# Kernel tuning notes

Measured on AMD Instinct MI355X. Metric: run time of the kernel, lower is better.

Reference implementation:

```python
import jax, jax.numpy as jnp
import numpy as np

SEQ, B, IN, H = 512, 256, 300, 256

def setup_inputs() -> dict:
    key = jax.random.key(0)
    ks = jax.random.split(key, 14)
    s = lambda *sh: 1.0 / np.sqrt(sh[0])
    inp = {
        'secuencia': jax.random.normal(ks[0], (SEQ, B, IN), jnp.float32),
        # RNN cell 1 (forward direction)
        'W1x': jax.random.normal(ks[1], (IN, H), jnp.float32) * s(IN),
        'W1h': jax.random.normal(ks[2], (H, H), jnp.float32) * s(H),
        'b1':  jax.random.normal(ks[3], (H,), jnp.float32) * 0.01,
        # RNN cell 2 (backward direction)
        'W2x': jax.random.normal(ks[4], (IN, H), jnp.float32) * s(IN),
        'W2h': jax.random.normal(ks[5], (H, H), jnp.float32) * s(H),
        'b2':  jax.random.normal(ks[6], (H,), jnp.float32) * 0.01,
        # MLP head (weights stored [in, out])
        'fc1_w': jax.random.normal(ks[7], (2 * H, 2 * H), jnp.float32) * s(2 * H),
        'fc1_b': jnp.zeros((2 * H,), jnp.float32),
        'fc2_w': jax.random.normal(ks[8], (2 * H, H), jnp.float32) * s(2 * H),
        'fc2_b': jnp.zeros((H,), jnp.float32),
        'fs_w':  jax.random.normal(ks[9], (H, 1), jnp.float32) * s(H),
        'fs_b':  jnp.zeros((1,), jnp.float32),
    }
    return inp

def _rnn_scan(seq, Wx, Wh, b):
    # seq: [S, B, IN] -> final hidden [B, H]; Elman cell h' = tanh(x Wx + h Wh + b)
    h0 = jnp.zeros((seq.shape[1], Wh.shape[0]), seq.dtype)
    def step(h, x):
        return jnp.tanh(x @ Wx + h @ Wh + b), None
    h_final, _ = jax.lax.scan(step, h0, seq)
    return h_final

def reference(secuencia, W1x, W1h, b1, W2x, W2h, b2,
              fc1_w, fc1_b, fc2_w, fc2_b, fs_w, fs_b):
    h1 = _rnn_scan(secuencia, W1x, W1h, b1)          # forward pass over time
    h2 = _rnn_scan(secuencia[::-1], W2x, W2h, b2)    # reversed pass over time
    h = jnp.concatenate([h1, h2], axis=1)            # [B, 2H]
    x = jax.nn.relu(h @ fc1_w + fc1_b)
    x = jax.nn.relu(x @ fc2_w + fc2_b)
    out = jnp.tanh(x @ fs_w + fs_b)                  # [B, 1]
    return out.squeeze()
```

## Files before the change

### kernel.cpp

```cpp
#include <hip/hip_runtime.h>

#define DI __device__ __forceinline__

typedef float f32x4 __attribute__((ext_vector_type(4)));
typedef float f4    __attribute__((ext_vector_type(4)));
typedef _Float16 h8 __attribute__((ext_vector_type(8)));
typedef _Float16 h4 __attribute__((ext_vector_type(4)));

#define SEQL 512
#define BATCH 256
#define INF 300
#define HID 256
#define N2 512
#define KP 320


DI float ftanh(float x) {
    float e = __builtin_amdgcn_exp2f(x * 2.8853900817779268f);
    return fmaf(-2.0f, __builtin_amdgcn_rcpf(e + 1.0f), 1.0f);
}

__global__ void prep_kernel(const float* __restrict__ W1x, const float* __restrict__ W2x,
                            const float* __restrict__ b1, const float* __restrict__ b2,
                            _Float16* __restrict__ WTs, float* __restrict__ bcat)
{
    int idx = blockIdx.x * 256 + threadIdx.x;
    if (idx < N2 * KP) {
        int j = idx / KP, z = idx - j * KP;
        int k = z ^ ((j & 7) << 3);
        float v = 0.f;
        if (k < INF) v = (j < HID) ? W1x[k * HID + j] : W2x[k * HID + (j - HID)];
        WTs[j * KP + z] = (_Float16)v;
    }
    if (idx < N2) bcat[idx] = (idx < HID) ? b1[idx] : b2[idx - HID];
}

__global__ __launch_bounds__(256, 2) void gemm_pre(
    const float* __restrict__ x, const _Float16* __restrict__ WTs,
    const float* __restrict__ bcat, _Float16* __restrict__ pre3)
{
    __shared__ _Float16 Ab[128 * 64];
    __shared__ _Float16 Bb[128 * 64];
    const int tid = threadIdx.x;
    const int w = tid >> 6, l = tid & 63;
    const int lj = l & 15, lg = l >> 4;
    const int bid = blockIdx.x;
    const int xcd = bid & 7;
    const int idx0 = bid >> 3;
    const int bn = idx0 & 3;
    const int bm = xcd * 128 + (idx0 >> 2);
    const size_t m0 = (size_t)bm * 128;
    const int j0b = bn * 128;
    const int wj = (w >> 1) * 64, wm2 = (w & 1) * 64;

    f32x4 acc[4][4];
#pragma unroll
    for (int a = 0; a < 4; ++a)
#pragma unroll
        for (int b = 0; b < 4; ++b) acc[a][b] = f32x4{0.f, 0.f, 0.f, 0.f};

    f4 bias4[4];
#pragma unroll
    for (int jt = 0; jt < 4; ++jt)
        bias4[jt] = *(const f4*)(bcat + j0b + wj + jt * 16 + lg * 4);

    for (int s = 0; s < 5; ++s) {
        const int k0 = s * 64;
#pragma unroll
        for (int q = 0; q < 4; ++q) {
            int idx = (w * 4 + q) * 64 + l;
            int jr = idx >> 3, sl = idx & 7;
            const _Float16* src = WTs + (size_t)(j0b + jr) * KP + k0 + sl * 8;
            _Float16* dst = &Bb[(w * 4 + q) * 512];
            __builtin_amdgcn_global_load_lds(
                (const __attribute__((address_space(1))) void*)src,
                (__attribute__((address_space(3))) void*)dst, 16, 0, 0);
        }
#pragma unroll
        for (int c = 0; c < 8; ++c) {
            int f = c * 256 + tid;
            int mr = f >> 4, k4 = f & 15;
            f4 v;
            if (k0 + k4 * 4 + 3 < INF)
                v = *(const f4*)(x + (m0 + mr) * INF + k0 + k4 * 4);
            else
                v = f4{0.f, 0.f, 0.f, 0.f};
            unsigned bo = (unsigned)mr * 128 + (((unsigned)k4 * 8) ^ ((mr & 7) << 4));
            *(h4*)((char*)Ab + bo) = h4{(_Float16)v[0], (_Float16)v[1], (_Float16)v[2], (_Float16)v[3]};
        }
        __syncthreads();
#pragma unroll
        for (int kk = 0; kk < 2; ++kk) {
            h8 aw[4], bx[4];
#pragma unroll
            for (int jt = 0; jt < 4; ++jt) {
                int jr = wj + jt * 16 + lj;
                unsigned bo = (unsigned)jr * 128 + (((unsigned)(kk * 64 + lg * 16)) ^ ((jr & 7) << 4));
                aw[jt] = *(const h8*)((const char*)Bb + bo);
            }
#pragma unroll
            for (int mt = 0; mt < 4; ++mt) {
                int mr = wm2 + mt * 16 + lj;
                unsigned bo = (unsigned)mr * 128 + (((unsigned)(kk * 64 + lg * 16)) ^ ((mr & 7) << 4));
                bx[mt] = *(const h8*)((const char*)Ab + bo);
            }
#pragma unroll
            for (int jt = 0; jt < 4; ++jt)
#pragma unroll
                for (int mt = 0; mt < 4; ++mt)
                    acc[jt][mt] = __builtin_amdgcn_mfma_f32_16x16x32_f16(aw[jt], bx[mt], acc[jt][mt], 0, 0, 0);
        }
        __syncthreads();
    }
    char* prc = (char*)pre3;
#pragma unroll
    for (int jt = 0; jt < 4; ++jt) {
        int slab = (j0b + wj + jt * 16) >> 4;
#pragma unroll
        for (int mt = 0; mt < 4; ++mt) {
            int M = (int)m0 + wm2 + mt * 16;
            size_t byte = (size_t)(M >> 8) * 262144 + (size_t)slab * 8192
                        + (size_t)((M & 255) + lj) * 32 + (size_t)lg * 8;
            h4 o;
#pragma unroll
            for (int i = 0; i < 4; ++i)
                o[i] = (_Float16)(acc[jt][mt][i] + bias4[jt][i]);
            *(h4*)(prc + byte) = o;
        }
    }
}

__global__ __launch_bounds__(512, 2) void rnn_scan(
    const float* __restrict__ W1h, const float* __restrict__ W2h,
    const _Float16* __restrict__ pre3, float* __restrict__ hcat)
{
    __shared__ char hbs[16384];
    char* hbc = hbs;
    const int tid = threadIdx.x;
    const int w = tid >> 6, l = tid & 63;
    const int lj = l & 15, lg = l >> 4;
    const int dir = blockIdx.x & 1;
    const int b0 = (int)(blockIdx.x >> 1) * 16;
    const float* Wh = dir ? W2h : W1h;
    const int j0 = w * 32;
    const int dirOff = dir ? HID : 0;

    h8 afrag[2][8];
#pragma unroll
    for (int jt = 0; jt < 2; ++jt) {
        int jc = j0 + jt * 16 + lj;
#pragma unroll
        for (int kk = 0; kk < 8; ++kk) {
            h8 t;
#pragma unroll
            for (int i = 0; i < 8; ++i) t[i] = (_Float16)Wh[(kk * 32 + lg * 8 + i) * HID + jc];
            afrag[jt][kk] = t;
        }
    }

    const unsigned rb = (unsigned)l * 16;
    const unsigned wb0 = (unsigned)w * 1024 + (unsigned)(lg >> 1) * 256
                       + (unsigned)lj * 16 + (unsigned)(lg & 1) * 8;

    ((h8*)hbs)[tid] = h8{0, 0, 0, 0, 0, 0, 0, 0};
    __syncthreads();

    const long long sb = dir ? -262144LL : 262144LL;
    const char* pp = (const char*)pre3 + (long long)(dir ? (SEQL - 1) : 0) * 262144
                   + (long long)dir * 131072
                   + (long long)w * 16384 + (long long)(b0 + lj) * 32 + lg * 8;
    h4 pA[2], pB[2];
#pragma unroll
    for (int jt = 0; jt < 2; ++jt) pA[jt] = *(const h4*)(pp + jt * 8192);
    pp += sb;
#pragma unroll
    for (int jt = 0; jt < 2; ++jt) pB[jt] = *(const h4*)(pp + jt * 8192);
    pp += sb;

#define RNN_STEP(RB, WB, P, DO_PF)                                                    \
    do {                                                                              \
        h8 bf[8];                                                                     \
        _Pragma("unroll")                                                             \
        for (int kk = 0; kk < 8; ++kk)                                                \
            bf[kk] = *(const h8*)(hbc + (RB) + kk * 1024 + rb);                       \
        f32x4 acc0, acc1;                                                             \
        _Pragma("unroll")                                                             \
        for (int i = 0; i < 4; ++i) { acc0[i] = (float)P[0][i]; acc1[i] = (float)P[1][i]; } \
        if (DO_PF) {                                                                  \
            P[0] = *(const h4*)(pp);                                                  \
            P[1] = *(const h4*)(pp + 8192);                                           \
            pp += sb;                                                                 \
        }                                                                             \
        _Pragma("unroll")                                                             \
        for (int kk = 0; kk < 8; ++kk)                                                \
            acc0 = __builtin_amdgcn_mfma_f32_16x16x32_f16(afrag[0][kk], bf[kk], acc0, 0, 0, 0); \
        h4 o0;                                                                        \
        _Pragma("unroll")                                                             \
        for (int i = 0; i < 4; ++i) o0[i] = (_Float16)ftanh(acc0[i]);                 \
        *(h4*)(hbc + (WB) + wb0) = o0;                                                \
        _Pragma("unroll")                                                             \
        for (int kk = 0; kk < 8; ++kk)                                                \
            acc1 = __builtin_amdgcn_mfma_f32_16x16x32_f16(afrag[1][kk], bf[kk], acc1, 0, 0, 0); \
        h4 o1;                                                                        \
        _Pragma("unroll")                                                             \
        for (int i = 0; i < 4; ++i) o1[i] = (_Float16)ftanh(acc1[i]);                 \
        *(h4*)(hbc + (WB) + wb0 + 512) = o1;                                          \
        __builtin_amdgcn_sched_barrier(0);                                            \
        asm volatile("s_waitcnt lgkmcnt(0)" ::: "memory");                            \
        __builtin_amdgcn_s_barrier();                                                 \
        __builtin_amdgcn_sched_barrier(0);                                            \
    } while (0)

    for (int tp = 0; tp < 255; ++tp) {
        RNN_STEP(0, 8192, pA, 1);
        RNN_STEP(8192, 0, pB, 1);
    }
    RNN_STEP(0, 8192, pA, 0);

    {
        f32x4 acc0, acc1;
#pragma unroll
        for (int i = 0; i < 4; ++i) { acc0[i] = (float)pB[0][i]; acc1[i] = (float)pB[1][i]; }
        h8 bf[8];
#pragma unroll
        for (int kk = 0; kk < 8; ++kk)
            bf[kk] = *(const h8*)(hbc + 8192 + kk * 1024 + rb);
#pragma unroll
        for (int kk = 0; kk < 8; ++kk) {
            acc0 = __builtin_amdgcn_mfma_f32_16x16x32_f16(afrag[0][kk], bf[kk], acc0, 0, 0, 0);
            acc1 = __builtin_amdgcn_mfma_f32_16x16x32_f16(afrag[1][kk], bf[kk], acc1, 0, 0, 0);
        }
        f4 v0, v1;
#pragma unroll
        for (int i = 0; i < 4; ++i) { v0[i] = ftanh(acc0[i]); v1[i] = ftanh(acc1[i]); }
        float* hc = hcat + (size_t)(b0 + lj) * N2 + dirOff + j0 + lg * 4;
        *(f4*)hc = v0;
        *(f4*)(hc + 16) = v1;
    }
#undef RNN_STEP
}

__global__ __launch_bounds__(256) void head_mlp(
    const float* __restrict__ hcat,
    const float* __restrict__ fc1w, const float* __restrict__ fc1b,
    const float* __restrict__ fc2w, const float* __restrict__ fc2b,
    const float* __restrict__ fsw, const float* __restrict__ fsb,
    float* __restrict__ out)
{
    __shared__ float hs[512];
    __shared__ float y1[512];
    __shared__ float red[4];
    const int b = blockIdx.x, tid = threadIdx.x;
    hs[tid] = hcat[(size_t)b * N2 + tid];
    hs[tid + 256] = hcat[(size_t)b * N2 + 256 + tid];
    __syncthreads();
    float a0 = fc1b[tid], a1 = fc1b[tid + 256];
#pragma unroll 8
    for (int k = 0; k < 512; ++k) {
        float h = hs[k];
        a0 = fmaf(h, fc1w[(size_t)k * 512 + tid], a0);
        a1 = fmaf(h, fc1w[(size_t)k * 512 + tid + 256], a1);
    }
    y1[tid] = fmaxf(a0, 0.f);
    y1[tid + 256] = fmaxf(a1, 0.f);
    __syncthreads();
    float c0 = fc2b[tid];
#pragma unroll 8
    for (int k = 0; k < 512; ++k) c0 = fmaf(y1[k], fc2w[(size_t)k * 256 + tid], c0);
    float p = fmaxf(c0, 0.f) * fsw[tid];
#pragma unroll
    for (int off = 32; off > 0; off >>= 1) p += __shfl_down(p, off);
    if ((tid & 63) == 0) red[tid >> 6] = p;
    __syncthreads();
    if (tid == 0) out[b] = ftanh(red[0] + red[1] + red[2] + red[3] + fsb[0]);
}

extern "C" void kernel_launch(void* const* d_in, const int* in_sizes, int n_in,
                              void* d_out, int out_size, void* d_ws, size_t ws_size,
                              hipStream_t stream)
{
    const float* x    = (const float*)d_in[0];
    const float* W1x  = (const float*)d_in[1];
    const float* W1h  = (const float*)d_in[2];
    const float* b1   = (const float*)d_in[3];
    const float* W2x  = (const float*)d_in[4];
    const float* W2h  = (const float*)d_in[5];
    const float* b2   = (const float*)d_in[6];
    const float* fc1w = (const float*)d_in[7];
    const float* fc1b = (const float*)d_in[8];
    const float* fc2w = (const float*)d_in[9];
    const float* fc2b = (const float*)d_in[10];
    const float* fsw  = (const float*)d_in[11];
    const float* fsb  = (const float*)d_in[12];

    char* ws = (char*)d_ws;
    size_t off = 0;
    _Float16* WTs = (_Float16*)(ws + off); off += (size_t)N2 * KP * sizeof(_Float16);
    float* bcat   = (float*)(ws + off);    off += (size_t)N2 * sizeof(float);
    float* hcat   = (float*)(ws + off);    off += (size_t)BATCH * N2 * sizeof(float);
    _Float16* pre3 = (_Float16*)(ws + off); off += (size_t)SEQL * BATCH * N2 * sizeof(_Float16);
    if (off > ws_size) return;

    prep_kernel<<<(N2 * KP + 255) / 256, 256, 0, stream>>>(W1x, W2x, b1, b2, WTs, bcat);
    gemm_pre<<<(SEQL * BATCH / 128) * (N2 / 128), 256, 0, stream>>>(x, WTs, bcat, pre3);
    rnn_scan<<<(BATCH / 16) * 2, 512, 0, stream>>>(W1h, W2h, pre3, hcat);
    head_mlp<<<BATCH, 256, 0, stream>>>(hcat, fc1w, fc1b, fc2w, fc2b, fsw, fsb, (float*)d_out);
}
```

Baseline: 483.9 us.

## Widen GEMM tile to 256 columns and batch four rows per head MLP block

The input-projection GEMM now uses 512-thread blocks covering 128 rows by 256 output columns, so each converted x tile is reused across twice as many columns and the fp32 x stream is read half as often. The grid drops from 4096 to 2048 blocks and LDS use per block grows. The bias load moves after the main loop to shorten register live ranges. The head MLP now handles four batch rows per block with one wavefront per row and vectorized weight loads, which cuts the number of times the fc weights are fetched by four, at the cost of fewer blocks (64).

Measured after the change: 493.5 us. Within noise of the previous version (+2.0%).

```diff
diff --git a/kernel.cpp b/kernel.cpp
--- a/kernel.cpp
+++ b/kernel.cpp
@@ -35,22 +35,22 @@
     if (idx < N2) bcat[idx] = (idx < HID) ? b1[idx] : b2[idx - HID];
 }
 
-__global__ __launch_bounds__(256, 2) void gemm_pre(
+__global__ __launch_bounds__(512, 2) void gemm_pre(
     const float* __restrict__ x, const _Float16* __restrict__ WTs,
     const float* __restrict__ bcat, _Float16* __restrict__ pre3)
 {
     __shared__ _Float16 Ab[128 * 64];
-    __shared__ _Float16 Bb[128 * 64];
+    __shared__ _Float16 Bb[256 * 64];
     const int tid = threadIdx.x;
     const int w = tid >> 6, l = tid & 63;
     const int lj = l & 15, lg = l >> 4;
     const int bid = blockIdx.x;
     const int xcd = bid & 7;
     const int idx0 = bid >> 3;
-    const int bn = idx0 & 3;
-    const int bm = xcd * 128 + (idx0 >> 2);
+    const int jn = idx0 & 1;
+    const int bm = xcd * 128 + (idx0 >> 1);
     const size_t m0 = (size_t)bm * 128;
-    const int j0b = bn * 128;
+    const int j0b = jn * 256;
     const int wj = (w >> 1) * 64, wm2 = (w & 1) * 64;
 
     f32x4 acc[4][4];
@@ -58,27 +58,22 @@
     for (int a = 0; a < 4; ++a)
 #pragma unroll
         for (int b = 0; b < 4; ++b) acc[a][b] = f32x4{0.f, 0.f, 0.f, 0.f};
-
-    f4 bias4[4];
-#pragma unroll
-    for (int jt = 0; jt < 4; ++jt)
-        bias4[jt] = *(const f4*)(bcat + j0b + wj + jt * 16 + lg * 4);
 
     for (int s = 0; s < 5; ++s) {
         const int k0 = s * 64;
 #pragma unroll
         for (int q = 0; q < 4; ++q) {
-            int idx = (w * 4 + q) * 64 + l;
+            int idx = q * 512 + tid;
             int jr = idx >> 3, sl = idx & 7;
             const _Float16* src = WTs + (size_t)(j0b + jr) * KP + k0 + sl * 8;
-            _Float16* dst = &Bb[(w * 4 + q) * 512];
+            _Float16* dst = &Bb[(q * 512 + w * 64) * 8];
             __builtin_amdgcn_global_load_lds(
                 (const __attribute__((address_space(1))) void*)src,
                 (__attribute__((address_space(3))) void*)dst, 16, 0, 0);
         }
 #pragma unroll
-        for (int c = 0; c < 8; ++c) {
-            int f = c * 256 + tid;
+        for (int c = 0; c < 4; ++c) {
+            int f = c * 512 + tid;
             int mr = f >> 4, k4 = f & 15;
             f4 v;
             if (k0 + k4 * 4 + 3 < INF)
@@ -112,6 +107,10 @@
         }
         __syncthreads();
     }
+    f4 bias4[4];
+#pragma unroll
+    for (int jt = 0; jt < 4; ++jt)
+        bias4[jt] = *(const f4*)(bcat + j0b + wj + jt * 16 + lg * 4);
     char* prc = (char*)pre3;
 #pragma unroll
     for (int jt = 0; jt < 4; ++jt) {
@@ -247,32 +246,61 @@
     const float* __restrict__ fsw, const float* __restrict__ fsb,
     float* __restrict__ out)
 {
-    __shared__ float hs[512];
-    __shared__ float y1[512];
-    __shared__ float red[4];
-    const int b = blockIdx.x, tid = threadIdx.x;
-    hs[tid] = hcat[(size_t)b * N2 + tid];
-    hs[tid + 256] = hcat[(size_t)b * N2 + 256 + tid];
+    __shared__ float hs[4 * 512];
+    __shared__ float y1[4 * 512];
+    __shared__ float y2[4 * 256];
+    const int tid = threadIdx.x;
+    const int b0 = blockIdx.x * 4;
+    const int r = tid >> 6;
+    const int lane = tid & 63;
+
+#pragma unroll
+    for (int c = 0; c < 2; ++c)
+        ((f4*)hs)[c * 256 + tid] = ((const f4*)(hcat + (size_t)b0 * N2))[c * 256 + tid];
     __syncthreads();
-    float a0 = fc1b[tid], a1 = fc1b[tid + 256];
-#pragma unroll 8
-    for (int k = 0; k < 512; ++k) {
-        float h = hs[k];
-        a0 = fmaf(h, fc1w[(size_t)k * 512 + tid], a0);
-        a1 = fmaf(h, fc1w[(size_t)k * 512 + tid + 256], a1);
-    }
-    y1[tid] = fmaxf(a0, 0.f);
-    y1[tid + 256] = fmaxf(a1, 0.f);
+
+    {
+        const int j0 = lane * 8;
+        f4 a0 = *(const f4*)(fc1b + j0);
+        f4 a1 = *(const f4*)(fc1b + j0 + 4);
+        for (int k = 0; k < 512; ++k) {
+            float h = hs[r * 512 + k];
+            f4 w0 = *(const f4*)(fc1w + (size_t)k * 512 + j0);
+            f4 w1 = *(const f4*)(fc1w + (size_t)k * 512 + j0 + 4);
+#pragma unroll
+            for (int i = 0; i < 4; ++i) { a0[i] = fmaf(h, w0[i], a0[i]); a1[i] = fmaf(h, w1[i], a1[i]); }
+        }
+#pragma unroll
+        for (int i = 0; i < 4; ++i) {
+            y1[r * 512 + j0 + i]     = fmaxf(a0[i], 0.f);
+            y1[r * 512 + j0 + 4 + i] = fmaxf(a1[i], 0.f);
+        }
+    }
     __syncthreads();
-    float c0 = fc2b[tid];
-#pragma unroll 8
-    for (int k = 0; k < 512; ++k) c0 = fmaf(y1[k], fc2w[(size_t)k * 256 + tid], c0);
-    float p = fmaxf(c0, 0.f) * fsw[tid];
-#pragma unroll
-    for (int off = 32; off > 0; off >>= 1) p += __shfl_down(p, off);
-    if ((tid & 63) == 0) red[tid >> 6] = p;
+
+    {
+        const int j2 = lane * 4;
+        f4 a = *(const f4*)(fc2b + j2);
+        for (int k = 0; k < 512; ++k) {
+            float yv = y1[r * 512 + k];
+            f4 w = *(const f4*)(fc2w + (size_t)k * 256 + j2);
+#pragma unroll
+            for (int i = 0; i < 4; ++i) a[i] = fmaf(yv, w[i], a[i]);
+        }
+#pragma unroll
+        for (int i = 0; i < 4; ++i) y2[r * 256 + j2 + i] = fmaxf(a[i], 0.f);
+    }
     __syncthreads();
-    if (tid == 0) out[b] = ftanh(red[0] + red[1] + red[2] + red[3] + fsb[0]);
+
+    {
+        float p = 0.f;
+#pragma unroll
+        for (int u = 0; u < 4; ++u)
+            p = fmaf(y2[r * 256 + lane + u * 64], fsw[lane + u * 64], p);
+#pragma unroll
+        for (int off = 32; off > 0; off >>= 1) p += __shfl_down(p, off);
+        if (lane == 0) out[b0 + r] = ftanh(p + fsb[0]);
+    }
 }
 
 extern "C" void kernel_launch(void* const* d_in, const int* in_sizes, int n_in,
@@ -302,7 +330,7 @@
     if (off > ws_size) return;
 
     prep_kernel<<<(N2 * KP + 255) / 256, 256, 0, stream>>>(W1x, W2x, b1, b2, WTs, bcat);
-    gemm_pre<<<(SEQL * BATCH / 128) * (N2 / 128), 256, 0, stream>>>(x, WTs, bcat, pre3);
+    gemm_pre<<<2048, 512, 0, stream>>>(x, WTs, bcat, pre3);
     rnn_scan<<<(BATCH / 16) * 2, 512, 0, stream>>>(W1h, W2h, pre3, hcat);
-    head_mlp<<<BATCH, 256, 0, stream>>>(hcat, fc1w, fc1b, fc2w, fc2b, fsw, fsb, (float*)d_out);
-}
+    head_mlp<<<64, 256, 0, stream>>>(hcat, fc1w, fc1b, fc2w, fc2b, fsw, fsb, (float*)d_out);
+}
```
